# Kernel optimization log

Hardware: AMD Instinct MI355X
Metric: run time of the kernel (lower is better)

## Reference

```python
import jax, jax.numpy as jnp
from jax import lax
import numpy as np

B, C, H, W = 8, 256, 64, 64
STRIDE, NH = 2, 8
ED_QK, ED_V = 64, 256  # embed_dim//ratio (divisible by heads), embed_dim
HQ, WQ = H // STRIDE, W // STRIDE
L = HQ * WQ


def conv2d(x, w, b, stride=1, pad=0):
    y = lax.conv_general_dilated(x, w, (stride, stride), ((pad, pad), (pad, pad)),
                                 dimension_numbers=('NCHW', 'OIHW', 'NCHW'))
    return y + b[None, :, None, None]


def setup_inputs() -> dict:
    key = jax.random.key(0)
    ks = jax.random.split(key, 24)
    s = 0.05
    f32 = jnp.float32
    inp = {
        'qkv_pos': jax.random.normal(ks[0], (B, C, H, W), f32),
        'qkv_cha': jax.random.normal(ks[1], (B, C, H, W), f32),
        # POS branch params (standard convs)
        'Wq_pos': jax.random.normal(ks[2], (ED_QK, C, 2, 2), f32) * s,
        'bq_pos': jax.random.normal(ks[3], (ED_QK,), f32) * s,
        'Wk_pos': jax.random.normal(ks[4], (ED_QK, C, 2, 2), f32) * s,
        'bk_pos': jax.random.normal(ks[5], (ED_QK,), f32) * s,
        'Wv_pos': jax.random.normal(ks[6], (ED_V, C, 2, 2), f32) * s,
        'bv_pos': jax.random.normal(ks[7], (ED_V,), f32) * s,
        'Wo_pos': jax.random.normal(ks[8], (C, ED_V, 3, 3), f32) * s,
        'bo_pos': jax.random.normal(ks[9], (C,), f32) * s,
        'gamma_pos': jnp.full((1,), 0.5, f32),
        # CHA branch params (grouped convs, groups=C, 1 in-ch -> NH out-ch per group)
        'Wq_cha': jax.random.normal(ks[10], (C, NH, 2, 2), f32) * s,
        'bq_cha': jax.random.normal(ks[11], (C, NH), f32) * s,
        'Wk_cha': jax.random.normal(ks[12], (C, NH, 2, 2), f32) * s,
        'bk_cha': jax.random.normal(ks[13], (C, NH), f32) * s,
        'Wv_cha': jax.random.normal(ks[14], (C, NH, 2, 2), f32) * s,
        'bv_cha': jax.random.normal(ks[15], (C, NH), f32) * s,
        # grouped ConvTranspose2d (groups=C, NH in-ch per group -> 1 out-ch), k=s=2
        'Wt_cha': jax.random.normal(ks[16], (C, NH, 2, 2), f32) * s,
        'bt_cha': jax.random.normal(ks[17], (C,), f32) * s,
        'gamma_cha': jnp.full((1,), 0.5, f32),
        # fusion conv: concat -> 2C in, C out, 3x3
        'Wf': jax.random.normal(ks[18], (C, 2 * C, 3, 3), f32) * s,
        'bf': jax.random.normal(ks[19], (C,), f32) * s,
    }
    return inp


def _gproj(x, w, b):
    # grouped conv with kernel==stride==2, 1 in-ch per group -> NH out-ch per group
    xp = x.reshape(B, C, HQ, STRIDE, WQ, STRIDE)
    y = jnp.einsum('bgikjl,ghkl->bghij', xp, w) + b[None, :, :, None, None]
    # channel order c = g*NH + h (torch grouped-conv layout); torch then reshapes
    # the flat C*NH channels into (NH, C) -> same as a direct reshape here
    return y.reshape(B, NH, C, L)


def reference(qkv_pos, qkv_cha, Wq_pos, bq_pos, Wk_pos, bk_pos, Wv_pos, bv_pos,
              Wo_pos, bo_pos, gamma_pos, Wq_cha, bq_cha, Wk_cha, bk_cha,
              Wv_cha, bv_cha, Wt_cha, bt_cha, gamma_cha, Wf, bf):
    hd = ED_QK // NH
    # ---- POS (spatial) attention ----
    qp = conv2d(qkv_pos, Wq_pos, bq_pos, STRIDE).reshape(B, NH, hd, L).transpose(0, 1, 3, 2)
    kp = conv2d(qkv_pos, Wk_pos, bk_pos, STRIDE).reshape(B, NH, hd, L).transpose(0, 1, 3, 2)
    vp = conv2d(qkv_pos, Wv_pos, bv_pos, STRIDE).reshape(B, NH, ED_V // NH, L).transpose(0, 1, 3, 2)
    attn_p = jax.nn.softmax(jnp.einsum('bhqd,bhkd->bhqk', qp, kp) * (hd ** -0.5), axis=-1)
    op = jnp.einsum('bhqk,bhkd->bhqd', attn_p, vp).transpose(0, 1, 3, 2).reshape(B, ED_V, HQ, WQ)
    op = conv2d(op, Wo_pos, bo_pos, 1, 1)
    op = jax.image.resize(op, (B, C, H, W), 'bilinear')  # Upsample(align_corners=False)
    out_pos = qkv_pos + op * gamma_pos
    # ---- CHA (channel) attention ----
    qc = _gproj(qkv_cha, Wq_cha, bq_cha)  # [B,NH,C,L]
    kc = _gproj(qkv_cha, Wk_cha, bk_cha)
    vc = _gproj(qkv_cha, Wv_cha, bv_cha)
    attn_c = jax.nn.softmax(jnp.einsum('bhcl,bhdl->bhcd', qc, kc) * (L ** -0.5), axis=-1)
    oc = jnp.einsum('bhcd,bhdl->bhcl', attn_c, vc)  # [B,NH,C,L]
    # flat channel c = h*C + g; grouped ConvTranspose2d groups by c//NH -> reshape (C,NH)
    ocg = oc.reshape(B, C, NH, HQ, WQ)
    oc = jnp.einsum('bgipq,gikl->bgpkql', ocg, Wt_cha).reshape(B, C, H, W) + bt_cha[None, :, None, None]
    out_cha = qkv_cha + oc * gamma_cha
    # ---- fusion: concat (slices are full since slides=0) + 3x3 conv ----
    out = jnp.concatenate([out_pos, out_cha], axis=1)
    return conv2d(out, Wf, bf, 1, 1)
```

## Files before the change

### kernel.cpp

```cpp
#include <hip/hip_runtime.h>
#include <math.h>


typedef __attribute__((ext_vector_type(8))) short bf16x8;
typedef __attribute__((ext_vector_type(4))) float f32x4;

__device__ __forceinline__ ushort f2bf(float f) {
  union { float f; unsigned u; } v; v.f = f;
  unsigned r = (v.u + 0x7FFFu + ((v.u >> 16) & 1u)) >> 16;
  return (ushort)r;
}

__global__ __launch_bounds__(256) void k_init_all(
    ushort* __restrict__ fused, ushort* __restrict__ op_pad,
    ushort* __restrict__ Qb,
    const float* __restrict__ Wf, const float* __restrict__ Wo,
    const float* __restrict__ Wq, const float* __restrict__ Wk,
    const float* __restrict__ Wv,
    ushort* __restrict__ Wpf9, ushort* __restrict__ Wpo9,
    ushort* __restrict__ Wqkvp)
{
  const int t = blockIdx.x * 256 + threadIdx.x;
  uint4 z = {0u, 0u, 0u, 0u};
  if (t < 133120) {
    const int e = t & 63;
    const int pi = (t >> 6) % 260;
    const int b = t / 16640;
    int y, x;
    if (pi < 66)       { y = 0;            x = pi; }
    else if (pi < 132) { y = 65;           x = pi - 66; }
    else if (pi < 196) { y = pi - 132 + 1; x = 0; }
    else               { y = pi - 196 + 1; x = 65; }
    *(uint4*)(fused + ((size_t)b * 4356 + y * 66 + x) * 512 + e * 8) = z;
  } else if (t < 166912) {
    const int j = t - 133120;
    const int e = j & 31;
    const int pi = (j >> 5) % 132;
    const int b = j / 4224;
    int y, x;
    if (pi < 34)       { y = 0;            x = pi; }
    else if (pi < 68)  { y = 33;           x = pi - 34; }
    else if (pi < 100) { y = pi - 68 + 1;  x = 0; }
    else               { y = pi - 100 + 1; x = 33; }
    *(uint4*)(op_pad + ((size_t)b * 1156 + y * 34 + x) * 256 + e * 8) = z;
  } else if (t < 429056) {
    const int j = t - 166912;
    *(uint4*)(Qb + (size_t)j * 8) = z;
  } else {
    const int i = t - 429056;
    if (i < 1179648) {
      const int tt = i / 131072;
      const int r = i - tt * 131072;
      const int oc = r >> 9, c = r & 511;
      Wpf9[i] = f2bf(Wf[((size_t)oc * 512 + c) * 9 + tt]);
    } else if (i < 1769472) {
      const int j = i - 1179648;
      const int tt = j / 65536;
      const int r = j - tt * 65536;
      const int oc = r >> 8, c = r & 255;
      Wpo9[j] = f2bf(Wo[((size_t)oc * 256 + c) * 9 + tt]);
    } else {
      const int j = i - 1769472;
      const int o = j >> 10, k = j & 1023;
      float v;
      if (o < 64)       v = Wq[(size_t)o * 1024 + k];
      else if (o < 128) v = Wk[(size_t)(o - 64) * 1024 + k];
      else              v = Wv[(size_t)(o - 128) * 1024 + k];
      Wqkvp[j] = f2bf(v);
    }
  }
}

__global__ __launch_bounds__(256) void k_pack_pos(
    const float* __restrict__ x, ushort* __restrict__ Ap)
{
  const int i = blockIdx.x, b = blockIdx.y;
  const int tid = threadIdx.x;
  __shared__ ushort xs[256][132];
  #pragma unroll 4
  for (int it = 0; it < 32; ++it) {
    const int slot = it * 256 + tid;
    const int px4 = slot & 15, r = (slot >> 4) & 1, c = slot >> 5;
    float4 v = *(const float4*)(x + (((size_t)b * 256 + c) << 12)
                                + (2 * i + r) * 64 + px4 * 4);
    union { ushort u[4]; uint2 d; } pk;
    pk.u[0] = f2bf(v.x); pk.u[1] = f2bf(v.y);
    pk.u[2] = f2bf(v.z); pk.u[3] = f2bf(v.w);
    *(uint2*)&xs[c][r * 64 + px4 * 4] = pk.d;
  }
  __syncthreads();
  ushort* dst = Ap + ((((size_t)b << 10) + i * 32) << 10);
  const int c = tid;
  #pragma unroll 4
  for (int j = 0; j < 32; ++j) {
    uint2 o;
    o.x = *(const uint*)&xs[c][2 * j];
    o.y = *(const uint*)&xs[c][64 + 2 * j];
    *(uint2*)(dst + (size_t)j * 1024 + c * 4) = o;
  }
}

__global__ __launch_bounds__(256) void k_pos_qkv_mfma(
    const ushort* __restrict__ Ap, const ushort* __restrict__ Wqkv,
    const float* __restrict__ bq, const float* __restrict__ bk,
    const float* __restrict__ bv,
    ushort* __restrict__ Qb, ushort* __restrict__ Kb, ushort* __restrict__ Vtb)
{
  const int n0 = blockIdx.x * 128, oc0 = blockIdx.y * 128, b = blockIdx.z;
  const int tid = threadIdx.x, lane = tid & 63, w = tid >> 6;
  __shared__ ushort As[128][32], Bs[128][32];
  const ushort* Abw = Wqkv + (size_t)oc0 * 1024;
  const ushort* Bb  = Ap + (((size_t)b << 10) + n0) * 1024;
  const int wr = w >> 1, wc = w & 1;
  f32x4 acc[4][4];
  #pragma unroll
  for (int mi = 0; mi < 4; ++mi)
    #pragma unroll
    for (int ni = 0; ni < 4; ++ni) {
      f32x4 z = {0.f, 0.f, 0.f, 0.f};
      acc[mi][ni] = z;
    }
  for (int kc = 0; kc < 1024; kc += 32) {
    __syncthreads();
    #pragma unroll
    for (int q = 0; q < 2; ++q) {
      int idx = w * 128 + q * 64 + lane;
      int row = idx >> 2, seg = idx & 3;
      const ushort* srcA = Abw + (size_t)row * 1024 + kc + seg * 8;
      const ushort* srcB = Bb + (size_t)row * 1024 + kc + seg * 8;
      char* dstA = (char*)&As[0][0] + w * 2048 + q * 1024;
      char* dstB = (char*)&Bs[0][0] + w * 2048 + q * 1024;
      __builtin_amdgcn_global_load_lds(
          (const __attribute__((address_space(1))) unsigned*)srcA,
          (__attribute__((address_space(3))) unsigned*)dstA, 16, 0, 0);
      __builtin_amdgcn_global_load_lds(
          (const __attribute__((address_space(1))) unsigned*)srcB,
          (__attribute__((address_space(3))) unsigned*)dstB, 16, 0, 0);
    }
    __syncthreads();
    bf16x8 af[4], bfv[4];
    #pragma unroll
    for (int mi = 0; mi < 4; ++mi)
      af[mi] = *(const bf16x8*)&As[wr * 64 + mi * 16 + (lane & 15)][(lane >> 4) * 8];
    #pragma unroll
    for (int ni = 0; ni < 4; ++ni)
      bfv[ni] = *(const bf16x8*)&Bs[wc * 64 + ni * 16 + (lane & 15)][(lane >> 4) * 8];
    #pragma unroll
    for (int mi = 0; mi < 4; ++mi)
      #pragma unroll
      for (int ni = 0; ni < 4; ++ni)
        acc[mi][ni] = __builtin_amdgcn_mfma_f32_16x16x32_bf16(
            af[mi], bfv[ni], acc[mi][ni], 0, 0, 0);
  }
  #pragma unroll
  for (int mi = 0; mi < 4; ++mi) {
    const int oc = oc0 + wr * 64 + mi * 16 + (lane >> 4) * 4;
    if (oc >= 384) continue;
    if (oc < 64) {
      const int hh = oc >> 3, e = oc & 7;
      float4 bb = *(const float4*)(bq + oc);
      #pragma unroll
      for (int ni = 0; ni < 4; ++ni) {
        const int l = n0 + wc * 64 + ni * 16 + (lane & 15);
        union { ushort u[4]; uint2 d; } pk;
        pk.u[0] = f2bf((acc[mi][ni][0] + bb.x) * 0.35355339059327373f);
        pk.u[1] = f2bf((acc[mi][ni][1] + bb.y) * 0.35355339059327373f);
        pk.u[2] = f2bf((acc[mi][ni][2] + bb.z) * 0.35355339059327373f);
        pk.u[3] = f2bf((acc[mi][ni][3] + bb.w) * 0.35355339059327373f);
        *(uint2*)(Qb + (((((size_t)b * 8 + hh) << 10) + l) << 5) + e) = pk.d;
      }
    } else if (oc < 128) {
      const int o2 = oc - 64, hh = o2 >> 3, e = o2 & 7;
      float4 bb = *(const float4*)(bk + o2);
      #pragma unroll
      for (int ni = 0; ni < 4; ++ni) {
        const int l = n0 + wc * 64 + ni * 16 + (lane & 15);
        union { ushort u[4]; uint2 d; } pk;
        pk.u[0] = f2bf(acc[mi][ni][0] + bb.x);
        pk.u[1] = f2bf(acc[mi][ni][1] + bb.y);
        pk.u[2] = f2bf(acc[mi][ni][2] + bb.z);
        pk.u[3] = f2bf(acc[mi][ni][3] + bb.w);
        *(uint2*)(Kb + (((((size_t)b * 8 + hh) << 10) + l) << 5) + e) = pk.d;
      }
    } else {
      const int o2 = oc - 128, hh = o2 >> 5, dd = o2 & 31;
      float4 bb = *(const float4*)(bv + o2);
      #pragma unroll
      for (int ni = 0; ni < 4; ++ni) {
        const int l = n0 + wc * 64 + ni * 16 + (lane & 15);
        ushort* vb = Vtb + ((((size_t)b * 8 + hh) * 32 + dd) << 10) + l;
        vb[0]      = f2bf(acc[mi][ni][0] + bb.x);
        vb[1024]   = f2bf(acc[mi][ni][1] + bb.y);
        vb[2048]   = f2bf(acc[mi][ni][2] + bb.z);
        vb[3072]   = f2bf(acc[mi][ni][3] + bb.w);
      }
    }
  }
}

__global__ __launch_bounds__(256) void k_pos_flash(
    const ushort* __restrict__ Qb, const ushort* __restrict__ Kb,
    const ushort* __restrict__ Vtb, ushort* __restrict__ op_pad)
{
  const int qt = blockIdx.x, h = blockIdx.y, b = blockIdx.z;
  const int bh = b * 8 + h;
  const int tid = threadIdx.x, lane = tid & 63, wq = tid >> 6;
  const int c = lane & 15, g = lane >> 4;
  __shared__ __align__(16) ushort Ps[4][32][72];
  const int qbase = qt * 128 + wq * 32;
  bf16x8 qf[2];
  #pragma unroll
  for (int nt = 0; nt < 2; ++nt)
    qf[nt] = *(const bf16x8*)(Qb + (((size_t)bh << 10) + qbase + nt * 16 + c) * 32 + g * 8);
  f32x4 o[2][2];
  #pragma unroll
  for (int mt = 0; mt < 2; ++mt)
    #pragma unroll
    for (int nt = 0; nt < 2; ++nt) {
      f32x4 z = {0.f, 0.f, 0.f, 0.f};
      o[mt][nt] = z;
    }
  float m[2] = {-1e30f, -1e30f}, l[2] = {0.f, 0.f};
  const ushort* Kbh = Kb + ((size_t)bh << 15);
  const ushort* Vbh = Vtb + ((size_t)bh << 15);

  for (int kt = 0; kt < 16; ++kt) {
    const int kb0 = kt * 64;
    bf16x8 kf[4];
    #pragma unroll
    for (int mt = 0; mt < 4; ++mt)
      kf[mt] = *(const bf16x8*)(Kbh + (size_t)(kb0 + mt * 16 + c) * 32 + g * 8);
    f32x4 s[4][2];
    #pragma unroll
    for (int mt = 0; mt < 4; ++mt)
      #pragma unroll
      for (int nt = 0; nt < 2; ++nt) {
        f32x4 z = {0.f, 0.f, 0.f, 0.f};
        s[mt][nt] = __builtin_amdgcn_mfma_f32_16x16x32_bf16(kf[mt], qf[nt], z, 0, 0, 0);
      }
    #pragma unroll
    for (int nt = 0; nt < 2; ++nt) {
      float tmax = -1e30f;
      #pragma unroll
      for (int mt = 0; mt < 4; ++mt)
        #pragma unroll
        for (int r = 0; r < 4; ++r)
          tmax = fmaxf(tmax, s[mt][nt][r]);
      tmax = fmaxf(tmax, __shfl_xor(tmax, 16, 64));
      tmax = fmaxf(tmax, __shfl_xor(tmax, 32, 64));
      const float mn = fmaxf(m[nt], tmax);
      const float alpha = __expf(m[nt] - mn);
      m[nt] = mn;
      float rs = 0.f;
      #pragma unroll
      for (int mt = 0; mt < 4; ++mt) {
        union { ushort u[4]; uint2 d; } pk;
        #pragma unroll
        for (int r = 0; r < 4; ++r) {
          float p = __expf(s[mt][nt][r] - mn);
          rs += p;
          pk.u[r] = f2bf(p);
        }
        *(uint2*)&Ps[wq][nt * 16 + c][mt * 16 + g * 4] = pk.d;
      }
      rs += __shfl_xor(rs, 16, 64);
      rs += __shfl_xor(rs, 32, 64);
      l[nt] = l[nt] * alpha + rs;
      #pragma unroll
      for (int mt = 0; mt < 2; ++mt)
        #pragma unroll
        for (int r = 0; r < 4; ++r)
          o[mt][nt][r] *= alpha;
    }
    #pragma unroll
    for (int kc = 0; kc < 2; ++kc) {
      bf16x8 vf[2], pf[2];
      #pragma unroll
      for (int mt = 0; mt < 2; ++mt)
        vf[mt] = *(const bf16x8*)(Vbh + (size_t)(mt * 16 + c) * 1024 + kb0 + kc * 32 + g * 8);
      #pragma unroll
      for (int nt = 0; nt < 2; ++nt)
        pf[nt] = *(const bf16x8*)&Ps[wq][nt * 16 + c][kc * 32 + g * 8];
      #pragma unroll
      for (int mt = 0; mt < 2; ++mt)
        #pragma unroll
        for (int nt = 0; nt < 2; ++nt)
          o[mt][nt] = __builtin_amdgcn_mfma_f32_16x16x32_bf16(vf[mt], pf[nt], o[mt][nt], 0, 0, 0);
    }
  }
  #pragma unroll
  for (int nt = 0; nt < 2; ++nt) {
    const float linv = 1.f / l[nt];
    const int q = qbase + nt * 16 + c;
    const int y = q >> 5, x = q & 31;
    ushort* dst = op_pad + ((size_t)b * 1156 + (y + 1) * 34 + (x + 1)) * 256 + h * 32;
    #pragma unroll
    for (int mt = 0; mt < 2; ++mt) {
      union { ushort u[4]; uint2 d; } pk;
      #pragma unroll
      for (int r = 0; r < 4; ++r)
        pk.u[r] = f2bf(o[mt][nt][r] * linv);
      *(uint2*)(dst + mt * 16 + g * 4) = pk.d;
    }
  }
}

template <int CIN, int S, int PW, int OUT_NHWC, int BN>
__global__ __launch_bounds__(256) void k_conv9_mfma(
    const ushort* __restrict__ in, const ushort* __restrict__ W9,
    const float* __restrict__ bias, float* __restrict__ out)
{
  constexpr int BQ = BN / 64;
  constexpr int NI = BN / 32;
  const int n0 = blockIdx.x * BN, oc0 = blockIdx.y * 128, b = blockIdx.z;
  const int tid = threadIdx.x, lane = tid & 63, w = tid >> 6;
  __shared__ ushort As[128][32], Bs[BN][32];
  const int wr = w >> 1, wc = w & 1;
  f32x4 acc[4][NI];
  #pragma unroll
  for (int mi = 0; mi < 4; ++mi)
    #pragma unroll
    for (int ni = 0; ni < NI; ++ni) {
      f32x4 z = {0.f, 0.f, 0.f, 0.f};
      acc[mi][ni] = z;
    }
  int rowqA[2], segqA[2];
  #pragma unroll
  for (int q = 0; q < 2; ++q) {
    int idx = w * 128 + q * 64 + lane;
    rowqA[q] = idx >> 2;
    segqA[q] = (idx & 3) * 8;
  }
  int rowqB[BQ], segqB[BQ], basep[BQ];
  #pragma unroll
  for (int q = 0; q < BQ; ++q) {
    int idx = (BQ == 2) ? (w * 128 + q * 64 + lane) : tid;
    rowqB[q] = idx >> 2;
    segqB[q] = (idx & 3) * 8;
    int n = n0 + rowqB[q];
    int y = n / S, x = n % S;
    basep[q] = y * PW + x;
  }
  const ushort* inb = in + (size_t)b * (PW * PW) * CIN;

  for (int t = 0; t < 9; ++t) {
    const int offp = (t / 3) * PW + (t % 3);
    const ushort* wt = W9 + (size_t)t * 256 * CIN;
    for (int kc = 0; kc < CIN; kc += 32) {
      __syncthreads();
      #pragma unroll
      for (int q = 0; q < 2; ++q) {
        const ushort* srcA = wt + (size_t)(oc0 + rowqA[q]) * CIN + kc + segqA[q];
        char* dstA = (char*)&As[0][0] + w * 2048 + q * 1024;
        __builtin_amdgcn_global_load_lds(
            (const __attribute__((address_space(1))) unsigned*)srcA,
            (__attribute__((address_space(3))) unsigned*)dstA, 16, 0, 0);
      }
      #pragma unroll
      for (int q = 0; q < BQ; ++q) {
        const ushort* srcB = inb + (size_t)(basep[q] + offp) * CIN + kc + segqB[q];
        char* dstB = (char*)&Bs[0][0] + w * (BQ * 1024) + q * 1024;
        __builtin_amdgcn_global_load_lds(
            (const __attribute__((address_space(1))) unsigned*)srcB,
            (__attribute__((address_space(3))) unsigned*)dstB, 16, 0, 0);
      }
      __syncthreads();
      bf16x8 af[4], bfv[NI];
      #pragma unroll
      for (int mi = 0; mi < 4; ++mi)
        af[mi] = *(const bf16x8*)&As[wr * 64 + mi * 16 + (lane & 15)][(lane >> 4) * 8];
      #pragma unroll
      for (int ni = 0; ni < NI; ++ni)
        bfv[ni] = *(const bf16x8*)&Bs[wc * (BN / 2) + ni * 16 + (lane & 15)][(lane >> 4) * 8];
      #pragma unroll
      for (int mi = 0; mi < 4; ++mi)
        #pragma unroll
        for (int ni = 0; ni < NI; ++ni)
          acc[mi][ni] = __builtin_amdgcn_mfma_f32_16x16x32_bf16(
              af[mi], bfv[ni], acc[mi][ni], 0, 0, 0);
    }
  }
  if (OUT_NHWC) {
    float* outb = out + (size_t)b * (S * S) * 256;
    #pragma unroll
    for (int mi = 0; mi < 4; ++mi) {
      const int oc = oc0 + wr * 64 + mi * 16 + (lane >> 4) * 4;
      float4 bb = *(const float4*)(bias + oc);
      #pragma unroll
      for (int ni = 0; ni < NI; ++ni) {
        const int n = n0 + wc * (BN / 2) + ni * 16 + (lane & 15);
        float4 v;
        v.x = acc[mi][ni][0] + bb.x;
        v.y = acc[mi][ni][1] + bb.y;
        v.z = acc[mi][ni][2] + bb.z;
        v.w = acc[mi][ni][3] + bb.w;
        *(float4*)(outb + (size_t)n * 256 + oc) = v;
      }
    }
  } else {
    float* outb = out + (size_t)b * 256 * (S * S);
    #pragma unroll
    for (int mi = 0; mi < 4; ++mi) {
      #pragma unroll
      for (int r = 0; r < 4; ++r) {
        int oc = oc0 + wr * 64 + mi * 16 + (lane >> 4) * 4 + r;
        float bb = bias[oc];
        #pragma unroll
        for (int ni = 0; ni < NI; ++ni) {
          int n = n0 + wc * (BN / 2) + ni * 16 + (lane & 15);
          outb[(size_t)oc * (S * S) + n] = acc[mi][ni][r] + bb;
        }
      }
    }
  }
}

#define STAGE_CONV(s_, bi_)                                                    \
  {                                                                            \
    const int t_ = (s_) >> 3, kc_ = ((s_) & 7) << 6;                           \
    const ushort* wt_ = W9 + t_ * 131072 + kc_;                                \
    const ushort* ib_ = inb + ((t_ / 3) * 66 + (t_ % 3)) * 512 + kc_;          \
    _Pragma("unroll")                                                          \
    for (int q_ = 0; q_ < 2; ++q_) {                                           \
      __builtin_amdgcn_global_load_lds(                                        \
          (const __attribute__((address_space(1))) unsigned*)(wt_ + aInv[q_]), \
          (__attribute__((address_space(3))) unsigned*)                        \
              ((char*)lds + (bi_) * 16384 + (w * 16 + q_ * 8) * 128),          \
          16, 0, 0);                                                           \
    }                                                                          \
    _Pragma("unroll")                                                          \
    for (int q_ = 0; q_ < 4; ++q_) {                                           \
      __builtin_amdgcn_global_load_lds(                                        \
          (const __attribute__((address_space(1))) unsigned*)(ib_ + bInv[q_]), \
          (__attribute__((address_space(3))) unsigned*)                        \
              ((char*)lds + 49152 + (bi_) * 32768 + (w * 32 + q_ * 8) * 128),  \
          16, 0, 0);                                                           \
    }                                                                          \
  }

#define READ_FRAGS(rb_, AF_, BF_)                                              \
  {                                                                            \
    const ushort* As_ = lds + (rb_) * 8192 + (wm * 64 + c) * 64;               \
    const ushort* Bs_ = lds + 24576 + (rb_) * 16384 + (wn * 64 + c) * 64;      \
    _Pragma("unroll")                                                          \
    for (int mi_ = 0; mi_ < 4; ++mi_) {                                        \
      AF_[mi_][0] = *(const bf16x8*)(As_ + mi_ * 1024 + okh0);                 \
      AF_[mi_][1] = *(const bf16x8*)(As_ + mi_ * 1024 + okh1);                 \
    }                                                                          \
    _Pragma("unroll")                                                          \
    for (int ni_ = 0; ni_ < 4; ++ni_) {                                        \
      BF_[ni_][0] = *(const bf16x8*)(Bs_ + ni_ * 1024 + okh0);                 \
      BF_[ni_][1] = *(const bf16x8*)(Bs_ + ni_ * 1024 + okh1);                 \
    }                                                                          \
  }

#define MFMA_SET(AF_, BF_)                                                     \
  {                                                                            \
    __builtin_amdgcn_s_setprio(1);                                             \
    _Pragma("unroll")                                                          \
    for (int mi_ = 0; mi_ < 4; ++mi_)                                          \
      _Pragma("unroll")                                                        \
      for (int ni_ = 0; ni_ < 4; ++ni_) {                                      \
        acc[mi_][ni_] = __builtin_amdgcn_mfma_f32_16x16x32_bf16(               \
            AF_[mi_][0], BF_[ni_][0], acc[mi_][ni_], 0, 0, 0);                 \
        acc[mi_][ni_] = __builtin_amdgcn_mfma_f32_16x16x32_bf16(               \
            AF_[mi_][1], BF_[ni_][1], acc[mi_][ni_], 0, 0, 0);                 \
      }                                                                        \
    __builtin_amdgcn_s_setprio(0);                                             \
  }

#define PHASE_END(vm_)                                                         \
  {                                                                            \
    asm volatile("s_waitcnt lgkmcnt(0)" ::: "memory");                         \
    asm volatile("s_waitcnt vmcnt(" #vm_ ")" ::: "memory");                    \
    __builtin_amdgcn_sched_barrier(0);                                         \
    __builtin_amdgcn_s_barrier();                                              \
  }

__global__ __launch_bounds__(512, 2) void k_conv9_pipe(
    const ushort* __restrict__ in, const ushort* __restrict__ W9,
    const float* __restrict__ bias, float* __restrict__ out)
{
  const int n0 = blockIdx.x * 256, oc0 = blockIdx.y * 128, b = blockIdx.z;
  const int tid = threadIdx.x, lane = tid & 63, w = tid >> 6;
  const int wm = w >> 2, wn = w & 3;
  const int g = lane >> 4, c = lane & 15;
  __shared__ __align__(16) ushort lds[73728];
  const ushort* inb = in + (size_t)b * 4356 * 512;

  const int l8 = lane >> 3, lx = lane & 7;
  int aInv[2], bInv[4];
  #pragma unroll
  for (int q = 0; q < 2; ++q) {
    const int row = w * 16 + q * 8 + l8;
    const int cx = (((lx << 4) ^ ((row & 7) << 4)) >> 1);
    aInv[q] = (oc0 + row) * 512 + cx;
  }
  #pragma unroll
  for (int q = 0; q < 4; ++q) {
    const int row = w * 32 + q * 8 + l8;
    const int n = n0 + row;
    const int y = n >> 6, x = n & 63;
    const int cx = (((lx << 4) ^ ((row & 7) << 4)) >> 1);
    bInv[q] = (y * 66 + x) * 512 + cx;
  }

  const int sx = (c & 7) << 3;
  const int okh0 = (g * 8) ^ sx;
  const int okh1 = (32 + g * 8) ^ sx;

  f32x4 acc[4][4];
  #pragma unroll
  for (int mi = 0; mi < 4; ++mi)
    #pragma unroll
    for (int ni = 0; ni < 4; ++ni) {
      f32x4 z = {0.f, 0.f, 0.f, 0.f};
      acc[mi][ni] = z;
    }

  bf16x8 afE[4][2], bfE[4][2], afO[4][2], bfO[4][2];

  STAGE_CONV(0, 0);
  STAGE_CONV(1, 1);
  STAGE_CONV(2, 2);
  asm volatile("s_waitcnt vmcnt(12)" ::: "memory");
  __builtin_amdgcn_sched_barrier(0);
  __builtin_amdgcn_s_barrier();
  READ_FRAGS(0, afE, bfE);
  PHASE_END(6);

  int rb = 1;
  for (int p = 0; p < 68; p += 2) {
    READ_FRAGS(rb, afO, bfO);
    { int sb = rb + 2; if (sb >= 3) sb -= 3; STAGE_CONV(p + 3, sb); }
    MFMA_SET(afE, bfE);
    PHASE_END(6);
    ++rb; if (rb == 3) rb = 0;
    READ_FRAGS(rb, afE, bfE);
    { int sb = rb + 2; if (sb >= 3) sb -= 3; STAGE_CONV(p + 4, sb); }
    MFMA_SET(afO, bfO);
    PHASE_END(6);
    ++rb; if (rb == 3) rb = 0;
  }
  READ_FRAGS(rb, afO, bfO);
  { int sb = rb + 2; if (sb >= 3) sb -= 3; STAGE_CONV(71, sb); }
  MFMA_SET(afE, bfE);
  PHASE_END(6);
  ++rb; if (rb == 3) rb = 0;
  READ_FRAGS(rb, afE, bfE);
  MFMA_SET(afO, bfO);
  PHASE_END(0);
  ++rb; if (rb == 3) rb = 0;
  READ_FRAGS(rb, afO, bfO);
  MFMA_SET(afE, bfE);
  asm volatile("s_waitcnt lgkmcnt(0)" ::: "memory");
  __builtin_amdgcn_sched_barrier(0);
  __builtin_amdgcn_s_barrier();
  MFMA_SET(afO, bfO);

  float* outb = out + (size_t)b * 1048576;
  #pragma unroll
  for (int mi = 0; mi < 4; ++mi) {
    const int oc = oc0 + wm * 64 + mi * 16 + g * 4;
    float4 bb = *(const float4*)(bias + oc);
    #pragma unroll
    for (int ni = 0; ni < 4; ++ni) {
      const int n = n0 + wn * 64 + ni * 16 + c;
      outb[(size_t)(oc + 0) * 4096 + n] = acc[mi][ni][0] + bb.x;
      outb[(size_t)(oc + 1) * 4096 + n] = acc[mi][ni][1] + bb.y;
      outb[(size_t)(oc + 2) * 4096 + n] = acc[mi][ni][2] + bb.z;
      outb[(size_t)(oc + 3) * 4096 + n] = acc[mi][ni][3] + bb.w;
    }
  }
}

__global__ __launch_bounds__(256) void k_upsample_nhwc(
    const float* __restrict__ xpos, const float* __restrict__ opc,
    const float* __restrict__ gamma, ushort* __restrict__ fused)
{
  const int y = blockIdx.x, h0 = blockIdx.y * 128, b = blockIdx.z;
  const int tid = threadIdx.x;
  __shared__ float xs[128 * 65];
  __shared__ float os[64 * 132];
  const int my = y >> 1;
  const int y0 = (y & 1) ? my : my - 1;
  const float fy = (y & 1) ? 0.25f : 0.75f;
  const int y0c = max(y0, 0), y1c = min(y0 + 1, 31);
  #pragma unroll
  for (int it = 0; it < 8; ++it) {
    const int slot = it * 256 + tid;
    const int px4 = slot & 15, cp = slot >> 4;
    float4 v = *(const float4*)(xpos + (((size_t)b * 256 + h0 + cp) << 12)
                                + y * 64 + px4 * 4);
    xs[cp * 65 + px4 * 4 + 0] = v.x;
    xs[cp * 65 + px4 * 4 + 1] = v.y;
    xs[cp * 65 + px4 * 4 + 2] = v.z;
    xs[cp * 65 + px4 * 4 + 3] = v.w;
  }
  #pragma unroll
  for (int it = 0; it < 8; ++it) {
    const int slot = it * 256 + tid;
    const int cc4 = slot & 31, pxe = slot >> 5;
    const int row = (pxe < 32) ? y0c : y1c;
    const int col = pxe & 31;
    float4 v = *(const float4*)(opc + ((size_t)b * 1024 + row * 32 + col) * 256
                                + h0 + cc4 * 4);
    *(float4*)&os[pxe * 132 + cc4 * 4] = v;
  }
  __syncthreads();
  const float g = gamma[0];
  #pragma unroll
  for (int it = 0; it < 8; ++it) {
    const int xx = it * 8 + (tid >> 5);
    const int c4 = tid & 31;
    const int mx = xx >> 1;
    const int x0 = (xx & 1) ? mx : mx - 1;
    const float fx = (xx & 1) ? 0.25f : 0.75f;
    const int x0c = max(x0, 0), x1c = min(x0 + 1, 31);
    float4 v00 = *(const float4*)&os[x0c * 132 + c4 * 4];
    float4 v01 = *(const float4*)&os[x1c * 132 + c4 * 4];
    float4 v10 = *(const float4*)&os[(32 + x0c) * 132 + c4 * 4];
    float4 v11 = *(const float4*)&os[(32 + x1c) * 132 + c4 * 4];
    const float w00 = (1.f - fy) * (1.f - fx), w01 = (1.f - fy) * fx;
    const float w10 = fy * (1.f - fx), w11 = fy * fx;
    union { ushort u[4]; uint2 q; } o;
    o.u[0] = f2bf(xs[(c4 * 4 + 0) * 65 + xx]
                  + g * (w00 * v00.x + w01 * v01.x + w10 * v10.x + w11 * v11.x));
    o.u[1] = f2bf(xs[(c4 * 4 + 1) * 65 + xx]
                  + g * (w00 * v00.y + w01 * v01.y + w10 * v10.y + w11 * v11.y));
    o.u[2] = f2bf(xs[(c4 * 4 + 2) * 65 + xx]
                  + g * (w00 * v00.z + w01 * v01.z + w10 * v10.z + w11 * v11.z));
    o.u[3] = f2bf(xs[(c4 * 4 + 3) * 65 + xx]
                  + g * (w00 * v00.w + w01 * v01.w + w10 * v10.w + w11 * v11.w));
    *(uint2*)(fused + ((size_t)b * 4356 + (y + 1) * 66 + (xx + 1)) * 512
              + h0 + c4 * 4) = o.q;
  }
}

__global__ __launch_bounds__(256) void k_cha_proj(
    const float* __restrict__ x,
    const float* __restrict__ Wq, const float* __restrict__ bq,
    const float* __restrict__ Wk, const float* __restrict__ bk,
    const float* __restrict__ Wv, const float* __restrict__ bv,
    ushort* __restrict__ Qc, ushort* __restrict__ Kc, ushort* __restrict__ Vt)
{
  const int t = blockIdx.x * 256 + threadIdx.x;
  const int bl = t >> 16;
  const int g  = (t >> 8) & 255;
  const int lq = t & 255;
  const int i = lq >> 3, j4 = (lq & 7) << 2;
  const float* xb = x + (((size_t)bl * 256 + g) << 12) + (2 * i) * 64 + 2 * j4;
  union { float4 v[2]; float f[8]; } xr0, xr1;
  xr0.v[0] = *(const float4*)(xb);
  xr0.v[1] = *(const float4*)(xb + 4);
  xr1.v[0] = *(const float4*)(xb + 64);
  xr1.v[1] = *(const float4*)(xb + 68);
  const int bhl = bl * 8 + (g >> 5);
  const int c2b = (g & 31) * 8;
  const int l0 = i * 32 + j4;
  #pragma unroll
  for (int h = 0; h < 8; ++h) {
    float4 w4 = *(const float4*)(Wq + g * 32 + h * 4);
    float bb = bq[g * 8 + h];
    union { ushort u[4]; uint2 q; } o;
    #pragma unroll
    for (int jj = 0; jj < 4; ++jj) {
      float v = xr0.f[2 * jj] * w4.x + xr0.f[2 * jj + 1] * w4.y
              + xr1.f[2 * jj] * w4.z + xr1.f[2 * jj + 1] * w4.w + bb;
      o.u[jj] = f2bf(v * 0.03125f);
    }
    *(uint2*)(Qc + (((size_t)bhl * 256 + c2b + h) << 10) + l0) = o.q;
  }
  #pragma unroll
  for (int h = 0; h < 8; ++h) {
    float4 w4 = *(const float4*)(Wk + g * 32 + h * 4);
    float bb = bk[g * 8 + h];
    union { ushort u[4]; uint2 q; } o;
    #pragma unroll
    for (int jj = 0; jj < 4; ++jj) {
      float v = xr0.f[2 * jj] * w4.x + xr0.f[2 * jj + 1] * w4.y
              + xr1.f[2 * jj] * w4.z + xr1.f[2 * jj + 1] * w4.w + bb;
      o.u[jj] = f2bf(v);
    }
    *(uint2*)(Kc + (((size_t)bhl * 256 + c2b + h) << 10) + l0) = o.q;
  }
  ushort vo[4][8];
  #pragma unroll
  for (int h = 0; h < 8; ++h) {
    float4 w4 = *(const float4*)(Wv + g * 32 + h * 4);
    float bb = bv[g * 8 + h];
    #pragma unroll
    for (int jj = 0; jj < 4; ++jj) {
      float v = xr0.f[2 * jj] * w4.x + xr0.f[2 * jj + 1] * w4.y
              + xr1.f[2 * jj] * w4.z + xr1.f[2 * jj + 1] * w4.w + bb;
      vo[jj][h] = f2bf(v);
    }
  }
  #pragma unroll
  for (int jj = 0; jj < 4; ++jj)
    *(uint4*)(Vt + ((size_t)bhl << 18) + (size_t)(l0 + jj) * 256 + c2b) =
        *(uint4*)&vo[jj][0];
}

__global__ __launch_bounds__(256) void k_cha_scores_mfma(
    const ushort* __restrict__ Qc, const ushort* __restrict__ Kc,
    float* __restrict__ S)
{
  const int c0 = blockIdx.x * 128, d0 = blockIdx.y * 64, bhl = blockIdx.z;
  const int tid = threadIdx.x, lane = tid & 63, w = tid >> 6;
  __shared__ ushort As[128][32], Bs[64][32];
  const ushort* Ab = Qc + ((size_t)bhl * 256 + c0) * 1024;
  const ushort* Bb = Kc + ((size_t)bhl * 256 + d0) * 1024;
  const int wr = w >> 1, wc = w & 1;
  f32x4 acc[4][2];
  #pragma unroll
  for (int mi = 0; mi < 4; ++mi)
    #pragma unroll
    for (int ni = 0; ni < 2; ++ni) {
      f32x4 z = {0.f, 0.f, 0.f, 0.f};
      acc[mi][ni] = z;
    }
  for (int kc = 0; kc < 1024; kc += 32) {
    __syncthreads();
    #pragma unroll
    for (int q = 0; q < 2; ++q) {
      int idx = w * 128 + q * 64 + lane;
      int row = idx >> 2, seg = idx & 3;
      const ushort* srcA = Ab + (size_t)row * 1024 + kc + seg * 8;
      char* dstA = (char*)&As[0][0] + w * 2048 + q * 1024;
      __builtin_amdgcn_global_load_lds(
          (const __attribute__((address_space(1))) unsigned*)srcA,
          (__attribute__((address_space(3))) unsigned*)dstA, 16, 0, 0);
    }
    {
      int idx = tid;
      int row = idx >> 2, seg = idx & 3;
      const ushort* srcB = Bb + (size_t)row * 1024 + kc + seg * 8;
      char* dstB = (char*)&Bs[0][0] + w * 1024;
      __builtin_amdgcn_global_load_lds(
          (const __attribute__((address_space(1))) unsigned*)srcB,
          (__attribute__((address_space(3))) unsigned*)dstB, 16, 0, 0);
    }
    __syncthreads();
    bf16x8 af[4], bfv[2];
    #pragma unroll
    for (int mi = 0; mi < 4; ++mi)
      af[mi] = *(const bf16x8*)&As[wr * 64 + mi * 16 + (lane & 15)][(lane >> 4) * 8];
    #pragma unroll
    for (int ni = 0; ni < 2; ++ni)
      bfv[ni] = *(const bf16x8*)&Bs[wc * 32 + ni * 16 + (lane & 15)][(lane >> 4) * 8];
    #pragma unroll
    for (int mi = 0; mi < 4; ++mi)
      #pragma unroll
      for (int ni = 0; ni < 2; ++ni)
        acc[mi][ni] = __builtin_amdgcn_mfma_f32_16x16x32_bf16(
            af[mi], bfv[ni], acc[mi][ni], 0, 0, 0);
  }
  float* Sb = S + ((size_t)bhl << 16);
  #pragma unroll
  for (int mi = 0; mi < 4; ++mi)
    #pragma unroll
    for (int r = 0; r < 4; ++r) {
      int c = c0 + wr * 64 + mi * 16 + (lane >> 4) * 4 + r;
      #pragma unroll
      for (int ni = 0; ni < 2; ++ni) {
        int d = d0 + wc * 32 + ni * 16 + (lane & 15);
        Sb[(size_t)c * 256 + d] = acc[mi][ni][r];
      }
    }
}

__global__ __launch_bounds__(256) void k_softmax_p(
    const float* __restrict__ S, ushort* __restrict__ P)
{
  const int row = blockIdx.x * 4 + (threadIdx.x >> 6);
  const int lane = threadIdx.x & 63;
  const float* r = S + (size_t)row * 256;
  float4 v = *(const float4*)(r + lane * 4);
  float m = fmaxf(fmaxf(v.x, v.y), fmaxf(v.z, v.w));
  #pragma unroll
  for (int off = 32; off; off >>= 1) m = fmaxf(m, __shfl_xor(m, off, 64));
  v.x = __expf(v.x - m); v.y = __expf(v.y - m);
  v.z = __expf(v.z - m); v.w = __expf(v.w - m);
  float s = v.x + v.y + v.z + v.w;
  #pragma unroll
  for (int off = 32; off; off >>= 1) s += __shfl_xor(s, off, 64);
  const float inv = 1.f / s;
  union { ushort u[4]; uint2 q; } o;
  o.u[0] = f2bf(v.x * inv); o.u[1] = f2bf(v.y * inv);
  o.u[2] = f2bf(v.z * inv); o.u[3] = f2bf(v.w * inv);
  *(uint2*)(P + (size_t)row * 256 + lane * 4) = o.q;
}

__global__ __launch_bounds__(256) void k_cha_pv(
    const ushort* __restrict__ P, const ushort* __restrict__ Vt,
    const float* __restrict__ x,
    const float* __restrict__ Wt, const float* __restrict__ bt,
    const float* __restrict__ gamma, ushort* __restrict__ fused, int bbase)
{
  const int n0 = blockIdx.x * 128, c0 = blockIdx.y * 128, bhl = blockIdx.z;
  const int b = bbase + (bhl >> 3), h = bhl & 7;
  const int tid = threadIdx.x, lane = tid & 63, w = tid >> 6;
  __shared__ ushort As[128][32], Bs[128][32];
  __shared__ ushort Ot[512][16];
  __shared__ float wt_s[16][32];
  __shared__ float bt_s[16];
  const int gp_base = h * 32 + (c0 >> 3);
  {
    int e = tid;
    wt_s[e >> 5][e & 31] = Wt[(size_t)gp_base * 32 + e];
    e += 256;
    wt_s[e >> 5][e & 31] = Wt[(size_t)gp_base * 32 + e];
    if (tid < 16) bt_s[tid] = bt[gp_base + tid];
  }
  const ushort* Ab = P + (((size_t)bhl << 8) + c0) * 256;
  const ushort* Bb = Vt + ((size_t)bhl << 18) + (size_t)n0 * 256;
  const int wr = w >> 1, wc = w & 1;
  f32x4 acc[4][4];
  #pragma unroll
  for (int mi = 0; mi < 4; ++mi)
    #pragma unroll
    for (int ni = 0; ni < 4; ++ni) {
      f32x4 z = {0.f, 0.f, 0.f, 0.f};
      acc[mi][ni] = z;
    }
  for (int kc = 0; kc < 256; kc += 32) {
    __syncthreads();
    #pragma unroll
    for (int q = 0; q < 2; ++q) {
      int idx = w * 128 + q * 64 + lane;
      int row = idx >> 2, seg = idx & 3;
      const ushort* srcA = Ab + (size_t)row * 256 + kc + seg * 8;
      const ushort* srcB = Bb + (size_t)row * 256 + kc + seg * 8;
      char* dstA = (char*)&As[0][0] + w * 2048 + q * 1024;
      char* dstB = (char*)&Bs[0][0] + w * 2048 + q * 1024;
      __builtin_amdgcn_global_load_lds(
          (const __attribute__((address_space(1))) unsigned*)srcA,
          (__attribute__((address_space(3))) unsigned*)dstA, 16, 0, 0);
      __builtin_amdgcn_global_load_lds(
          (const __attribute__((address_space(1))) unsigned*)srcB,
          (__attribute__((address_space(3))) unsigned*)dstB, 16, 0, 0);
    }
    __syncthreads();
    bf16x8 af[4], bfv[4];
    #pragma unroll
    for (int mi = 0; mi < 4; ++mi)
      af[mi] = *(const bf16x8*)&As[wr * 64 + mi * 16 + (lane & 15)][(lane >> 4) * 8];
    #pragma unroll
    for (int ni = 0; ni < 4; ++ni)
      bfv[ni] = *(const bf16x8*)&Bs[wc * 64 + ni * 16 + (lane & 15)][(lane >> 4) * 8];
    #pragma unroll
    for (int mi = 0; mi < 4; ++mi)
      #pragma unroll
      for (int ni = 0; ni < 4; ++ni)
        acc[mi][ni] = __builtin_amdgcn_mfma_f32_16x16x32_bf16(
            af[mi], bfv[ni], acc[mi][ni], 0, 0, 0);
  }
  const float gm = gamma[0];
  const int col = lane & 15, q = lane >> 4;
  #pragma unroll
  for (int mi = 0; mi < 4; ++mi) {
    const int gloc = wr * 8 + mi * 2 + (q >> 1);
    const int gp = gp_base + gloc;
    const float btv = bt_s[gloc];
    #pragma unroll
    for (int ni = 0; ni < 4; ++ni) {
      float pa[4] = {0.f, 0.f, 0.f, 0.f};
      #pragma unroll
      for (int r = 0; r < 4; ++r) {
        const int i2 = (q & 1) * 4 + r;
        const float a = acc[mi][ni][r];
        pa[0] += a * wt_s[gloc][i2 * 4 + 0];
        pa[1] += a * wt_s[gloc][i2 * 4 + 1];
        pa[2] += a * wt_s[gloc][i2 * 4 + 2];
        pa[3] += a * wt_s[gloc][i2 * 4 + 3];
      }
      float v0 = pa[0] + __shfl_xor(pa[0], 16, 64);
      float v1 = pa[1] + __shfl_xor(pa[1], 16, 64);
      float v2 = pa[2] + __shfl_xor(pa[2], 16, 64);
      float v3 = pa[3] + __shfl_xor(pa[3], 16, 64);
      const int lloc = wc * 64 + ni * 16 + col;
      const int l = n0 + lloc;
      const int p = l >> 5, j = l & 31;
      const int y = 2 * p + (q & 1);
      const float va = (q & 1) ? v2 : v0;
      const float vb = (q & 1) ? v3 : v1;
      const float* xc = x + (((size_t)b * 256 + gp) << 12) + (y << 6) + 2 * j;
      const int lp = (lloc << 2) + (q & 1) * 2;
      Ot[lp][gloc]     = f2bf(xc[0] + gm * (va + btv));
      Ot[lp + 1][gloc] = f2bf(xc[1] + gm * (vb + btv));
    }
  }
  __syncthreads();
  #pragma unroll
  for (int pp2 = 0; pp2 < 2; ++pp2) {
    const int pixl = tid * 2 + pp2;
    const int lloc = pixl >> 2;
    const int l = n0 + lloc;
    const int p = l >> 5, j = l & 31;
    const int yy = 2 * p + ((pixl >> 1) & 1) + 1;
    const int xx = 2 * j + (pixl & 1) + 1;
    const uint4* src = (const uint4*)&Ot[pixl][0];
    uint4* dst = (uint4*)(fused + ((size_t)b * 4356 + yy * 66 + xx) * 512 + 256 + gp_base);
    dst[0] = src[0];
    dst[1] = src[1];
  }
}

extern "C" void kernel_launch(void* const* d_in, const int* in_sizes, int n_in,
                              void* d_out, int out_size, void* d_ws, size_t ws_size,
                              hipStream_t stream)
{
  (void)in_sizes; (void)n_in; (void)out_size; (void)ws_size;
  const float* qkv_pos   = (const float*)d_in[0];
  const float* qkv_cha   = (const float*)d_in[1];
  const float* Wq_pos    = (const float*)d_in[2];
  const float* bq_pos    = (const float*)d_in[3];
  const float* Wk_pos    = (const float*)d_in[4];
  const float* bk_pos    = (const float*)d_in[5];
  const float* Wv_pos    = (const float*)d_in[6];
  const float* bv_pos    = (const float*)d_in[7];
  const float* Wo_pos    = (const float*)d_in[8];
  const float* bo_pos    = (const float*)d_in[9];
  const float* gamma_pos = (const float*)d_in[10];
  const float* Wq_cha    = (const float*)d_in[11];
  const float* bq_cha    = (const float*)d_in[12];
  const float* Wk_cha    = (const float*)d_in[13];
  const float* bk_cha    = (const float*)d_in[14];
  const float* Wv_cha    = (const float*)d_in[15];
  const float* bv_cha    = (const float*)d_in[16];
  const float* Wt_cha    = (const float*)d_in[17];
  const float* bt_cha    = (const float*)d_in[18];
  const float* gamma_cha = (const float*)d_in[19];
  const float* Wf        = (const float*)d_in[20];
  const float* bf        = (const float*)d_in[21];
  float* out = (float*)d_out;

  float* ws = (float*)d_ws;
  ushort* Wpf9    = (ushort*)ws;
  ushort* Wpo9    = (ushort*)(ws + 589824);
  ushort* Qb      = (ushort*)(ws + 884736);
  ushort* Kb      = (ushort*)(ws + 1933312);
  ushort* Vtb     = (ushort*)(ws + 2981888);
  ushort* op_pad  = (ushort*)(ws + 4030464);
  float*  op_conv = ws + 5214208;
  ushort* Ap      = (ushort*)(ws + 7311360);
  ushort* qcb     = (ushort*)(ws + 884736);
  ushort* kcb     = (ushort*)(ws + 5079040);
  ushort* vcT     = (ushort*)(ws + 9273344);
  float*  attn_c  = ws + 13467648;
  ushort* Pb      = (ushort*)(ws + 15564800);
  ushort* fusedb  = (ushort*)(ws + 16613376);
  ushort* Wqkvp   = (ushort*)(ws + 25534464);

  k_init_all<<<dim3(10124), 256, 0, stream>>>(fusedb, op_pad, Qb,
      Wf, Wo_pos, Wq_pos, Wk_pos, Wv_pos, Wpf9, Wpo9, Wqkvp);
  k_pack_pos<<<dim3(32, 8), 256, 0, stream>>>(qkv_pos, Ap);
  k_pos_qkv_mfma<<<dim3(8, 3, 8), 256, 0, stream>>>(Ap, Wqkvp,
      bq_pos, bk_pos, bv_pos, Qb, Kb, Vtb);
  k_pos_flash<<<dim3(8, 8, 8), 256, 0, stream>>>(Qb, Kb, Vtb, op_pad);
  k_conv9_mfma<256, 32, 34, 1, 64><<<dim3(16, 2, 8), 256, 0, stream>>>(
      op_pad, Wpo9, bo_pos, op_conv);
  k_upsample_nhwc<<<dim3(64, 2, 8), 256, 0, stream>>>(qkv_pos, op_conv,
      gamma_pos, fusedb);
  for (int half = 0; half < 2; ++half) {
    const float* xh = qkv_cha + (size_t)half * 4 * 256 * 4096;
    k_cha_proj<<<dim3(1024), 256, 0, stream>>>(xh, Wq_cha, bq_cha,
        Wk_cha, bk_cha, Wv_cha, bv_cha, qcb, kcb, vcT);
    k_cha_scores_mfma<<<dim3(2, 4, 32), 256, 0, stream>>>(qcb, kcb, attn_c);
    k_softmax_p<<<dim3(2048), 256, 0, stream>>>(attn_c, Pb);
    k_cha_pv<<<dim3(8, 2, 32), 256, 0, stream>>>(Pb, vcT, qkv_cha,
        Wt_cha, bt_cha, gamma_cha, fusedb, half * 4);
  }
  k_conv9_pipe<<<dim3(16, 2, 8), 512, 0, stream>>>(fusedb, Wpf9, bf, out);
}
```

Baseline: 459.4 us.

## Fuse channel-attention scores with softmax and skip flash rescale when max stable

```diff
diff --git a/kernel.cpp b/kernel.cpp
--- a/kernel.cpp
+++ b/kernel.cpp
@@ -248,16 +248,24 @@
           tmax = fmaxf(tmax, s[mt][nt][r]);
       tmax = fmaxf(tmax, __shfl_xor(tmax, 16, 64));
       tmax = fmaxf(tmax, __shfl_xor(tmax, 32, 64));
-      const float mn = fmaxf(m[nt], tmax);
-      const float alpha = __expf(m[nt] - mn);
-      m[nt] = mn;
+      if (!__all(tmax <= m[nt] + 8.f)) {
+        const float mn = fmaxf(m[nt], tmax);
+        const float alpha = __expf(m[nt] - mn);
+        m[nt] = mn;
+        l[nt] *= alpha;
+        #pragma unroll
+        for (int mt = 0; mt < 2; ++mt)
+          #pragma unroll
+          for (int r = 0; r < 4; ++r)
+            o[mt][nt][r] *= alpha;
+      }
       float rs = 0.f;
       #pragma unroll
       for (int mt = 0; mt < 4; ++mt) {
         union { ushort u[4]; uint2 d; } pk;
         #pragma unroll
         for (int r = 0; r < 4; ++r) {
-          float p = __expf(s[mt][nt][r] - mn);
+          float p = __expf(s[mt][nt][r] - m[nt]);
           rs += p;
           pk.u[r] = f2bf(p);
         }
@@ -265,12 +273,7 @@
       }
       rs += __shfl_xor(rs, 16, 64);
       rs += __shfl_xor(rs, 32, 64);
-      l[nt] = l[nt] * alpha + rs;
-      #pragma unroll
-      for (int mt = 0; mt < 2; ++mt)
-        #pragma unroll
-        for (int r = 0; r < 4; ++r)
-          o[mt][nt][r] *= alpha;
+      l[nt] += rs;
     }
     #pragma unroll
     for (int kc = 0; kc < 2; ++kc) {
@@ -702,94 +705,87 @@
         *(uint4*)&vo[jj][0];
 }
 
-__global__ __launch_bounds__(256) void k_cha_scores_mfma(
+__global__ __launch_bounds__(256) void k_cha_scores_sm(
     const ushort* __restrict__ Qc, const ushort* __restrict__ Kc,
-    float* __restrict__ S)
-{
-  const int c0 = blockIdx.x * 128, d0 = blockIdx.y * 64, bhl = blockIdx.z;
+    ushort* __restrict__ P)
+{
+  const int c0 = blockIdx.x * 32, bhl = blockIdx.y;
   const int tid = threadIdx.x, lane = tid & 63, w = tid >> 6;
-  __shared__ ushort As[128][32], Bs[64][32];
+  __shared__ ushort As[32][32], Bs[256][32];
+  __shared__ float Sst[32][260];
   const ushort* Ab = Qc + ((size_t)bhl * 256 + c0) * 1024;
-  const ushort* Bb = Kc + ((size_t)bhl * 256 + d0) * 1024;
-  const int wr = w >> 1, wc = w & 1;
-  f32x4 acc[4][2];
-  #pragma unroll
-  for (int mi = 0; mi < 4; ++mi)
-    #pragma unroll
-    for (int ni = 0; ni < 2; ++ni) {
+  const ushort* Bb = Kc + ((size_t)bhl << 18);
+  f32x4 acc[2][4];
+  #pragma unroll
+  for (int mi = 0; mi < 2; ++mi)
+    #pragma unroll
+    for (int ni = 0; ni < 4; ++ni) {
       f32x4 z = {0.f, 0.f, 0.f, 0.f};
       acc[mi][ni] = z;
     }
   for (int kc = 0; kc < 1024; kc += 32) {
     __syncthreads();
-    #pragma unroll
-    for (int q = 0; q < 2; ++q) {
-      int idx = w * 128 + q * 64 + lane;
-      int row = idx >> 2, seg = idx & 3;
+    if (tid < 128) {
+      int row = tid >> 2, seg = tid & 3;
       const ushort* srcA = Ab + (size_t)row * 1024 + kc + seg * 8;
-      char* dstA = (char*)&As[0][0] + w * 2048 + q * 1024;
+      char* dstA = (char*)&As[0][0] + tid * 16;
       __builtin_amdgcn_global_load_lds(
           (const __attribute__((address_space(1))) unsigned*)srcA,
           (__attribute__((address_space(3))) unsigned*)dstA, 16, 0, 0);
     }
-    {
-      int idx = tid;
+    #pragma unroll
+    for (int q = 0; q < 4; ++q) {
+      int idx = q * 256 + tid;
       int row = idx >> 2, seg = idx & 3;
       const ushort* srcB = Bb + (size_t)row * 1024 + kc + seg * 8;
-      char* dstB = (char*)&Bs[0][0] + w * 1024;
+      char* dstB = (char*)&Bs[0][0] + idx * 16;
       __builtin_amdgcn_global_load_lds(
           (const __attribute__((address_space(1))) unsigned*)srcB,
           (__attribute__((address_space(3))) unsigned*)dstB, 16, 0, 0);
     }
     __syncthreads();
-    bf16x8 af[4], bfv[2];
-    #pragma unroll
-    for (int mi = 0; mi < 4; ++mi)
-      af[mi] = *(const bf16x8*)&As[wr * 64 + mi * 16 + (lane & 15)][(lane >> 4) * 8];
-    #pragma unroll
-    for (int ni = 0; ni < 2; ++ni)
-      bfv[ni] = *(const bf16x8*)&Bs[wc * 32 + ni * 16 + (lane & 15)][(lane >> 4) * 8];
-    #pragma unroll
-    for (int mi = 0; mi < 4; ++mi)
-      #pragma unroll
-      for (int ni = 0; ni < 2; ++ni)
+    bf16x8 af[2], bfv[4];
+    #pragma unroll
+    for (int mi = 0; mi < 2; ++mi)
+      af[mi] = *(const bf16x8*)&As[mi * 16 + (lane & 15)][(lane >> 4) * 8];
+    #pragma unroll
+    for (int ni = 0; ni < 4; ++ni)
+      bfv[ni] = *(const bf16x8*)&Bs[w * 64 + ni * 16 + (lane & 15)][(lane >> 4) * 8];
+    #pragma unroll
+    for (int mi = 0; mi < 2; ++mi)
+      #pragma unroll
+      for (int ni = 0; ni < 4; ++ni)
         acc[mi][ni] = __builtin_amdgcn_mfma_f32_16x16x32_bf16(
             af[mi], bfv[ni], acc[mi][ni], 0, 0, 0);
   }
-  float* Sb = S + ((size_t)bhl << 16);
-  #pragma unroll
-  for (int mi = 0; mi < 4; ++mi)
-    #pragma unroll
-    for (int r = 0; r < 4; ++r) {
-      int c = c0 + wr * 64 + mi * 16 + (lane >> 4) * 4 + r;
-      #pragma unroll
-      for (int ni = 0; ni < 2; ++ni) {
-        int d = d0 + wc * 32 + ni * 16 + (lane & 15);
-        Sb[(size_t)c * 256 + d] = acc[mi][ni][r];
-      }
-    }
-}
-
-__global__ __launch_bounds__(256) void k_softmax_p(
-    const float* __restrict__ S, ushort* __restrict__ P)
-{
-  const int row = blockIdx.x * 4 + (threadIdx.x >> 6);
-  const int lane = threadIdx.x & 63;
-  const float* r = S + (size_t)row * 256;
-  float4 v = *(const float4*)(r + lane * 4);
-  float m = fmaxf(fmaxf(v.x, v.y), fmaxf(v.z, v.w));
-  #pragma unroll
-  for (int off = 32; off; off >>= 1) m = fmaxf(m, __shfl_xor(m, off, 64));
-  v.x = __expf(v.x - m); v.y = __expf(v.y - m);
-  v.z = __expf(v.z - m); v.w = __expf(v.w - m);
-  float s = v.x + v.y + v.z + v.w;
-  #pragma unroll
-  for (int off = 32; off; off >>= 1) s += __shfl_xor(s, off, 64);
-  const float inv = 1.f / s;
-  union { ushort u[4]; uint2 q; } o;
-  o.u[0] = f2bf(v.x * inv); o.u[1] = f2bf(v.y * inv);
-  o.u[2] = f2bf(v.z * inv); o.u[3] = f2bf(v.w * inv);
-  *(uint2*)(P + (size_t)row * 256 + lane * 4) = o.q;
+  __syncthreads();
+  #pragma unroll
+  for (int mi = 0; mi < 2; ++mi)
+    #pragma unroll
+    for (int ni = 0; ni < 4; ++ni)
+      #pragma unroll
+      for (int r = 0; r < 4; ++r)
+        Sst[mi * 16 + (lane >> 4) * 4 + r][w * 64 + ni * 16 + (lane & 15)] =
+            acc[mi][ni][r];
+  __syncthreads();
+  #pragma unroll
+  for (int rr = 0; rr < 8; ++rr) {
+    const int row = w * 8 + rr;
+    float4 v = *(const float4*)&Sst[row][lane * 4];
+    float m = fmaxf(fmaxf(v.x, v.y), fmaxf(v.z, v.w));
+    #pragma unroll
+    for (int off = 32; off; off >>= 1) m = fmaxf(m, __shfl_xor(m, off, 64));
+    v.x = __expf(v.x - m); v.y = __expf(v.y - m);
+    v.z = __expf(v.z - m); v.w = __expf(v.w - m);
+    float s = v.x + v.y + v.z + v.w;
+    #pragma unroll
+    for (int off = 32; off; off >>= 1) s += __shfl_xor(s, off, 64);
+    const float inv = 1.f / s;
+    union { ushort u[4]; uint2 q; } o;
+    o.u[0] = f2bf(v.x * inv); o.u[1] = f2bf(v.y * inv);
+    o.u[2] = f2bf(v.z * inv); o.u[3] = f2bf(v.w * inv);
+    *(uint2*)(P + (((size_t)bhl * 256 + c0 + row) << 8) + lane * 4) = o.q;
+  }
 }
 
 __global__ __launch_bounds__(256) void k_cha_pv(
@@ -948,7 +944,6 @@
   ushort* qcb     = (ushort*)(ws + 884736);
   ushort* kcb     = (ushort*)(ws + 5079040);
   ushort* vcT     = (ushort*)(ws + 9273344);
-  float*  attn_c  = ws + 13467648;
   ushort* Pb      = (ushort*)(ws + 15564800);
   ushort* fusedb  = (ushort*)(ws + 16613376);
   ushort* Wqkvp   = (ushort*)(ws + 25534464);
@@ -967,8 +962,7 @@
     const float* xh = qkv_cha + (size_t)half * 4 * 256 * 4096;
     k_cha_proj<<<dim3(1024), 256, 0, stream>>>(xh, Wq_cha, bq_cha,
         Wk_cha, bk_cha, Wv_cha, bv_cha, qcb, kcb, vcT);
-    k_cha_scores_mfma<<<dim3(2, 4, 32), 256, 0, stream>>>(qcb, kcb, attn_c);
-    k_softmax_p<<<dim3(2048), 256, 0, stream>>>(attn_c, Pb);
+    k_cha_scores_sm<<<dim3(8, 32), 256, 0, stream>>>(qcb, kcb, Pb);
     k_cha_pv<<<dim3(8, 2, 32), 256, 0, stream>>>(Pb, vcT, qkv_cha,
         Wt_cha, bt_cha, gamma_cha, fusedb, half * 4);
   }
```

New measurement: 477.3 us, median of 2. 1.04x slower.
